# Performance work log

Hardware: AMD Instinct MI355X
Metric: run time of the kernel (lower is better)

The kernel has to match this reference:

```python
import jax, jax.numpy as jnp
import numpy as np
import math

S = 300      # seq_len (timesteps)
P = 10       # n_players
ED = 20      # embedding_dim
D = 512      # d_model = mlp_layers[-1]
H = 8        # nhead
L = 4        # num_layers
FF = 2048    # dim_feedforward
NPID = 600
NPL, NBL, NSL = 121, 1331, 10


def setup_inputs() -> dict:
    key = jax.random.key(0)
    ks = iter(jax.random.split(key, 64))

    def rn(shape, s=0.05):
        return jax.random.normal(next(ks), shape, dtype=jnp.float32) * s

    inp = {
        "player_xs": rn((S, P), 1.0),
        "player_ys": rn((S, P), 1.0),
        "player_hoop_sides": jax.random.uniform(next(ks), (S, P), dtype=jnp.float32),
        "ball_xs": rn((S,), 1.0),
        "ball_ys": rn((S,), 1.0),
        "ball_zs": rn((S,), 1.0),
        "emb_table": rn((NPID, ED)),
        "ball_emb": rn((ED,)),
        "cls_emb": rn((D,)),
        "pW0": rn((128, ED + 3)), "pb0": rn((128,)),
        "pW1": rn((256, 128)), "pb1": rn((256,)),
        "pW2": rn((D, 256)), "pb2": rn((D,)),
        "bW0": rn((128, ED + 3)), "bb0": rn((128,)),
        "bW1": rn((256, 128)), "bb1": rn((256,)),
        "bW2": rn((D, 256)), "bb2": rn((D,)),
        "Wqkv": rn((L, 3 * D, D)), "bqkv": rn((L, 3 * D)),
        "Wo": rn((L, D, D)), "bo": rn((L, D)),
        "W1f": rn((L, FF, D)), "b1f": rn((L, FF)),
        "W2f": rn((L, D, FF)), "b2f": rn((L, D)),
        "g1": jnp.ones((L, D), jnp.float32), "be1": jnp.zeros((L, D), jnp.float32),
        "g2": jnp.ones((L, D), jnp.float32), "be2": jnp.zeros((L, D), jnp.float32),
        "cpW": rn((NPL, D)), "cpb": jnp.zeros((NPL,), jnp.float32),
        "cbW": rn((NBL, D)), "cbb": jnp.zeros((NBL,), jnp.float32),
        "csW": rn((NSL, D)), "csb": jnp.zeros((NSL,), jnp.float32),
        "player_idxs": jax.random.randint(next(ks), (S, P), 0, NPID),
    }
    return inp


def _ln(x, g, b):
    m = x.mean(-1, keepdims=True)
    v = ((x - m) ** 2).mean(-1, keepdims=True)
    return (x - m) / jnp.sqrt(v + 1e-5) * g + b


def _mlp(x, W0, b0, W1, b1, W2, b2):
    x = jax.nn.relu(x @ W0.T + b0)
    x = jax.nn.relu(x @ W1.T + b1)
    return x @ W2.T + b2


def reference(player_xs, player_ys, player_hoop_sides, ball_xs, ball_ys, ball_zs,
              emb_table, ball_emb, cls_emb,
              pW0, pb0, pW1, pb1, pW2, pb2,
              bW0, bb0, bW1, bb1, bW2, bb2,
              Wqkv, bqkv, Wo, bo, W1f, b1f, W2f, b2f,
              g1, be1, g2, be2,
              cpW, cpb, cbW, cbb, csW, csb,
              player_idxs):
    scale = math.sqrt(D)
    # player tokens: [S*P, D]
    pe = emb_table[player_idxs.reshape(-1)]  # sigmoid == "none"
    pin = jnp.concatenate([pe,
                           player_xs.reshape(-1, 1),
                           player_ys.reshape(-1, 1),
                           player_hoop_sides.reshape(-1, 1)], axis=1)
    pf = _mlp(pin, pW0, pb0, pW1, pb1, pW2, pb2) * scale
    # ball tokens: [S, D]
    bin_ = jnp.concatenate([jnp.broadcast_to(ball_emb, (S, ED)),
                            ball_xs[:, None], ball_ys[:, None], ball_zs[:, None]], axis=1)
    bf = _mlp(bin_, bW0, bb0, bW1, bb1, bW2, bb2) * scale
    # [S*P + S + S, D] = [3600, D]
    x = jnp.concatenate([pf, bf, jnp.broadcast_to(cls_emb, (S, D))], axis=0)

    # growing block-causal mask: token j visible to token i iff step(j) <= step(i)
    steps = jnp.concatenate([jnp.repeat(jnp.arange(S), P), jnp.arange(S), jnp.arange(S)])
    mask = jnp.where(steps[None, :] <= steps[:, None], 0.0, -jnp.inf).astype(x.dtype)

    hd = D // H
    sc = 1.0 / math.sqrt(hd)
    for l in range(L):  # post-norm TransformerEncoderLayer, relu activation, dropout=0
        qkv = x @ Wqkv[l].T + bqkv[l]
        q, k, v = jnp.split(qkv, 3, axis=1)
        q = q.reshape(-1, H, hd)
        k = k.reshape(-1, H, hd)
        v = v.reshape(-1, H, hd)
        att = jnp.einsum('qhd,khd->hqk', q, k) * sc + mask
        att = jax.nn.softmax(att, axis=-1)
        o = jnp.einsum('hqk,khd->qhd', att, v).reshape(-1, D)
        x = _ln(x + o @ Wo[l].T + bo[l], g1[l], be1[l])
        ff = jax.nn.relu(x @ W1f[l].T + b1f[l]) @ W2f[l].T + b2f[l]
        x = _ln(x + ff, g2[l], be2[l])

    return (x @ cpW.T + cpb, x @ cbW.T + cbb, x @ csW.T + csb)
```

## Files before the change

### kernel.cpp

```cpp
#include <hip/hip_runtime.h>
#include <hip/hip_bf16.h>

typedef unsigned short u16;
typedef unsigned int u32;
typedef __attribute__((ext_vector_type(8))) short bf16x8;
typedef __attribute__((ext_vector_type(4))) float f32x4;

#define T_TOK 3600
#define D_    512
#define H_    8
#define HD    64
#define NKT   57
#define NQT   113
#define VT_S  3648
#define KSPLIT 8
#define ZSLICE 1843200
#define SQRT512 22.627416997969522f
#define QK_SCALE 0.18033688011112042f

__device__ __forceinline__ u16 f2bf(float f) {
    unsigned int x = __float_as_uint(f);
    unsigned int lsb = (x >> 16) & 1;
    return (u16)((x + 0x7fffu + lsb) >> 16);
}
__device__ __forceinline__ float bf2f(u16 u) {
    return __uint_as_float(((unsigned int)u) << 16);
}
__device__ __forceinline__ u32 cvt_pk_bf16(float a, float b) {
    u32 r;
    asm("v_cvt_pk_bf16_f32 %0, %1, %2" : "=v"(r) : "v"(a), "v"(b));
    return r;
}
__device__ __forceinline__ void async_ld16(const void* g, void* l) {
    __builtin_amdgcn_global_load_lds(
        (const __attribute__((address_space(1))) void*)g,
        (__attribute__((address_space(3))) void*)l, 16, 0, 0);
}
__device__ __forceinline__ int step_of(int i) {
    return (i < 3000) ? (i / 10) : ((i < 3300) ? (i - 3000) : (i - 3300));
}
__device__ __forceinline__ void tile_minmax(int kbase, int& mn, int& mx) {
    int a = kbase, b = min(kbase + 63, T_TOK - 1);
    mn = 0x7fffffff; mx = -1;
    if (a < 3000)              { mn = min(mn, a / 10);              mx = max(mx, min(b, 2999) / 10); }
    if (b >= 3000 && a < 3300) { mn = min(mn, max(a, 3000) - 3000); mx = max(mx, min(b, 3299) - 3000); }
    if (b >= 3300)             { mn = min(mn, max(a, 3300) - 3300); mx = max(mx, b - 3300); }
}

__global__ __launch_bounds__(256) void gather_kernel(
    const float* __restrict__ pxs, const float* __restrict__ pys, const float* __restrict__ phs,
    const float* __restrict__ bxs, const float* __restrict__ bys, const float* __restrict__ bzs,
    const float* __restrict__ emb_table, const float* __restrict__ ball_emb,
    const float* __restrict__ cls_emb, const int* __restrict__ pidx,
    float* __restrict__ IN, float* __restrict__ x, u16* __restrict__ xb)
{
    int g = blockIdx.x * 256 + threadIdx.x;
    if (g < 3300) {
        float* row = IN + g * 24;
        if (g < 3000) {
            int id = pidx[g];
            #pragma unroll
            for (int e = 0; e < 20; e++) row[e] = emb_table[id * 20 + e];
            row[20] = pxs[g]; row[21] = pys[g]; row[22] = phs[g];
        } else {
            int b = g - 3000;
            #pragma unroll
            for (int e = 0; e < 20; e++) row[e] = ball_emb[e];
            row[20] = bxs[b]; row[21] = bys[b]; row[22] = bzs[b];
        }
        row[23] = 0.f;
    }
    for (int i = g; i < 300 * 512; i += 3840) {
        float v = cls_emb[i & 511];
        x[3300 * 512 + i] = v;
        xb[3300 * 512 + i] = f2bf(v);
    }
}

__global__ __launch_bounds__(256) void w2b4_kernel(
    const float* __restrict__ s0, const float* __restrict__ s1,
    const float* __restrict__ s2, const float* __restrict__ s3,
    u16* __restrict__ dst)
{
    int stride = gridDim.x * 256;
    for (int i = blockIdx.x * 256 + threadIdx.x; i < 786432; i += stride) {
        const float4* src;
        int j = i;
        if (j < 196608)      { src = (const float4*)s0; }
        else if (j < 262144) { src = (const float4*)s1; j -= 196608; }
        else if (j < 524288) { src = (const float4*)s2; j -= 262144; }
        else                 { src = (const float4*)s3; j -= 524288; }
        float4 v = src[j];
        ushort4 o;
        o.x = f2bf(v.x); o.y = f2bf(v.y); o.z = f2bf(v.z); o.w = f2bf(v.w);
        reinterpret_cast<ushort4*>(dst)[i] = o;
    }
}

__global__ __launch_bounds__(256) void w2bh_kernel(
    const float* __restrict__ cp, const float* __restrict__ cb,
    const float* __restrict__ cs, const float* __restrict__ bp,
    const float* __restrict__ bb, const float* __restrict__ bs,
    u16* __restrict__ dst, float* __restrict__ bias)
{
    int stride = gridDim.x * 256;
    for (int i = blockIdx.x * 256 + threadIdx.x; i < 187136; i += stride) {
        const float4* src;
        int j = i;
        if (j < 15488)       { src = (const float4*)cp; }
        else if (j < 185856) { src = (const float4*)cb; j -= 15488; }
        else                 { src = (const float4*)cs; j -= 185856; }
        float4 v = src[j];
        ushort4 o;
        o.x = f2bf(v.x); o.y = f2bf(v.y); o.z = f2bf(v.z); o.w = f2bf(v.w);
        reinterpret_cast<ushort4*>(dst)[i] = o;
    }
    int g = blockIdx.x * 256 + threadIdx.x;
    if (g < 1462)
        bias[g] = (g < 121) ? bp[g] : (g < 1452) ? bb[g - 121] : bs[g - 1452];
}

__device__ __forceinline__ void stage_f32(
    const float* __restrict__ src, int nrows, int K, int lda,
    int r0, int kk, int srow, int scg, u16* dst)
{
    u16 tmp[16];
    int rr = r0 + srow;
    if (rr < nrows) {
        if (((lda & 3) == 0) && (kk + scg + 16 <= K)) {
            const float4* p = reinterpret_cast<const float4*>(src + (size_t)rr * lda + kk + scg);
            #pragma unroll
            for (int q = 0; q < 4; q++) {
                float4 v = p[q];
                tmp[q*4+0] = f2bf(v.x); tmp[q*4+1] = f2bf(v.y);
                tmp[q*4+2] = f2bf(v.z); tmp[q*4+3] = f2bf(v.w);
            }
        } else {
            #pragma unroll
            for (int e = 0; e < 16; e++) {
                int kc = kk + scg + e;
                tmp[e] = (kc < K) ? f2bf(src[(size_t)rr * lda + kc]) : (u16)0;
            }
        }
    } else {
        #pragma unroll
        for (int e = 0; e < 16; e++) tmp[e] = 0;
    }
    *reinterpret_cast<bf16x8*>(dst)     = *reinterpret_cast<const bf16x8*>(&tmp[0]);
    *reinterpret_cast<bf16x8*>(dst + 8) = *reinterpret_cast<const bf16x8*>(&tmp[8]);
}

template<int RELU, int DUAL>
__global__ __launch_bounds__(256) void gemm_tok(
    const float* __restrict__ A0, const float* __restrict__ W0p,
    const float* __restrict__ b0p, float* __restrict__ C0,
    const float* __restrict__ A1, const float* __restrict__ W1p,
    const float* __restrict__ b1p, float* __restrict__ C1,
    u16* __restrict__ Cb,
    int M0, int M1, int N, int K, int lda, float scale)
{
    int zz = blockIdx.z;
    int M = zz ? M1 : M0;
    int m0 = blockIdx.x * 128;
    if (m0 >= M) return;
    const float* A = zz ? A1 : A0;
    const float* W = zz ? W1p : W0p;
    const float* bias = zz ? b1p : b0p;
    float* C = zz ? C1 : C0;
    u16* CbL = DUAL ? (zz ? Cb + (size_t)M0 * N : Cb) : nullptr;

    __shared__ u16 As[128][40];
    __shared__ u16 Bs[128][40];
    int t = threadIdx.x;
    int w = t >> 6, l = t & 63;
    int ll = l & 15, lg = l >> 4;
    int wr = w >> 1, wc = w & 1;
    int n0 = blockIdx.y * 128;
    int srow = t >> 1;
    int scg  = (t & 1) * 16;

    f32x4 acc[4][4];
    #pragma unroll
    for (int i = 0; i < 4; i++)
        #pragma unroll
        for (int j = 0; j < 4; j++) acc[i][j] = (f32x4){0.f, 0.f, 0.f, 0.f};

    for (int kk = 0; kk < K; kk += 32) {
        stage_f32(A, M, K, lda, m0, kk, srow, scg, &As[srow][scg]);
        stage_f32(W, N, K, K, n0, kk, srow, scg, &Bs[srow][scg]);
        __syncthreads();
        bf16x8 af[4], bf[4];
        #pragma unroll
        for (int i = 0; i < 4; i++)
            af[i] = *reinterpret_cast<const bf16x8*>(&As[wr*64 + i*16 + ll][lg*8]);
        #pragma unroll
        for (int j = 0; j < 4; j++)
            bf[j] = *reinterpret_cast<const bf16x8*>(&Bs[wc*64 + j*16 + ll][lg*8]);
        #pragma unroll
        for (int i = 0; i < 4; i++)
            #pragma unroll
            for (int j = 0; j < 4; j++)
                acc[i][j] = __builtin_amdgcn_mfma_f32_16x16x32_bf16(af[i], bf[j], acc[i][j], 0, 0, 0);
        __syncthreads();
    }

    float bv[4];
    #pragma unroll
    for (int j = 0; j < 4; j++) {
        int n = n0 + wc*64 + j*16 + ll;
        bv[j] = (n < N) ? bias[n] : 0.f;
    }
    #pragma unroll
    for (int i = 0; i < 4; i++) {
        #pragma unroll
        for (int r = 0; r < 4; r++) {
            int m = m0 + wr*64 + i*16 + lg*4 + r;
            if (m >= M) continue;
            #pragma unroll
            for (int j = 0; j < 4; j++) {
                int n = n0 + wc*64 + j*16 + ll;
                if (n >= N) continue;
                float v = acc[i][j][r] + bv[j];
                if (RELU) v = fmaxf(v, 0.f);
                v *= scale;
                C[(size_t)m * N + n] = v;
                if (DUAL) CbL[(size_t)m * N + n] = f2bf(v);
            }
        }
    }
}

template<int RELU, int BF16OUT, int QSCALE, int SPLITK, int HEADS>
__global__ __launch_bounds__(256) void gemm_async(
    const u16* __restrict__ A, const u16* __restrict__ W,
    const float* __restrict__ bias, void* __restrict__ Cv, float* __restrict__ C1,
    int M, int N, int K, int lda, float scale)
{
    __shared__ u16 As[4096];
    __shared__ u16 Bs[4096];
    int t = threadIdx.x;
    int w = t >> 6, l = t & 63;
    int ll = l & 15, lg = l >> 4;
    int wr = w >> 1, wc = w & 1;
    int m0 = blockIdx.x * 128, n0 = blockIdx.y * 128;
    int srow = l >> 2;
    int skg  = (l & 3) * 8;
    int kz = SPLITK ? blockIdx.z : 0;
    int khalf = SPLITK ? (K >> 1) : K;
    int kbeg = kz * khalf;

    const u16* pa0 = A + (size_t)min(m0 + w * 16 + srow, M - 1) * lda + skg;
    const u16* pa1 = A + (size_t)min(m0 + 64 + w * 16 + srow, M - 1) * lda + skg;
    const u16* pb0 = W + (size_t)min(n0 + w * 16 + srow, N - 1) * K + skg;
    const u16* pb1 = W + (size_t)min(n0 + 64 + w * 16 + srow, N - 1) * K + skg;
    u16* la0 = &As[(w * 16) * 32];
    u16* la1 = &As[(64 + w * 16) * 32];
    u16* lb0 = &Bs[(w * 16) * 32];
    u16* lb1 = &Bs[(64 + w * 16) * 32];

    f32x4 acc[4][4];
    #pragma unroll
    for (int i = 0; i < 4; i++)
        #pragma unroll
        for (int j = 0; j < 4; j++) acc[i][j] = (f32x4){0.f, 0.f, 0.f, 0.f};

    for (int kk = kbeg; kk < kbeg + khalf; kk += 32) {
        async_ld16(pa0 + kk, la0);
        async_ld16(pa1 + kk, la1);
        async_ld16(pb0 + kk, lb0);
        async_ld16(pb1 + kk, lb1);
        __syncthreads();
        bf16x8 af[4], bf[4];
        #pragma unroll
        for (int i = 0; i < 4; i++)
            af[i] = *reinterpret_cast<const bf16x8*>(&As[(wr*64 + i*16 + ll) * 32 + lg*8]);
        #pragma unroll
        for (int j = 0; j < 4; j++)
            bf[j] = *reinterpret_cast<const bf16x8*>(&Bs[(wc*64 + j*16 + ll) * 32 + lg*8]);
        #pragma unroll
        for (int i = 0; i < 4; i++)
            #pragma unroll
            for (int j = 0; j < 4; j++)
                acc[i][j] = __builtin_amdgcn_mfma_f32_16x16x32_bf16(af[i], bf[j], acc[i][j], 0, 0, 0);
        __syncthreads();
    }

    float bv[4];
    #pragma unroll
    for (int j = 0; j < 4; j++) {
        int n = n0 + wc*64 + j*16 + ll;
        bv[j] = (n < N && (!SPLITK || kz == 0)) ? bias[n] : 0.f;
    }
    #pragma unroll
    for (int i = 0; i < 4; i++) {
        #pragma unroll
        for (int r = 0; r < 4; r++) {
            int m = m0 + wr*64 + i*16 + lg*4 + r;
            if (m >= M) continue;
            #pragma unroll
            for (int j = 0; j < 4; j++) {
                int n = n0 + wc*64 + j*16 + ll;
                if (n >= N) continue;
                float v = acc[i][j][r] + bv[j];
                if (RELU) v = fmaxf(v, 0.f);
                v *= scale;
                if (QSCALE && n < 512) v *= QK_SCALE;
                if (HEADS) {
                    float* o = (float*)Cv;
                    if (n < 121)       o[(size_t)m * 121 + n] = v;
                    else if (n < 1452) (o + 435600)[(size_t)m * 1331 + (n - 121)] = v;
                    else               (o + 5227200)[(size_t)m * 10 + (n - 1452)] = v;
                } else if (SPLITK && kz == 1) {
                    C1[(size_t)m * N + n] = v;
                } else if (BF16OUT) {
                    ((u16*)Cv)[(size_t)m * N + n] = f2bf(v);
                } else {
                    ((float*)Cv)[(size_t)m * N + n] = v;
                }
            }
        }
    }
}

__global__ __launch_bounds__(256) void vtrans_kernel(
    const u16* __restrict__ qkvb, u16* __restrict__ vt)
{
    __shared__ u16 tile[64][72];
    int t = threadIdx.x;
    int tok0 = blockIdx.x * 64;
    int h = blockIdx.y;
    {
        int i = t >> 2, c16 = (t & 3) * 16;
        int tok = tok0 + i;
        bf16x8 a = {}, b = {};
        if (tok < T_TOK) {
            const bf16x8* p = reinterpret_cast<const bf16x8*>(qkvb + (size_t)tok * 1536 + 1024 + h * HD + c16);
            a = p[0]; b = p[1];
        }
        *reinterpret_cast<bf16x8*>(&tile[i][c16])     = a;
        *reinterpret_cast<bf16x8*>(&tile[i][c16 + 8]) = b;
    }
    __syncthreads();
    {
        int d = t >> 2, i0 = (t & 3) * 16;
        u16 tt[16];
        #pragma unroll
        for (int e = 0; e < 16; e++) tt[e] = tile[i0 + e][d];
        u16* dst = vt + (size_t)(h * HD + d) * VT_S + tok0 + i0;
        *reinterpret_cast<bf16x8*>(dst)     = *reinterpret_cast<const bf16x8*>(&tt[0]);
        *reinterpret_cast<bf16x8*>(dst + 8) = *reinterpret_cast<const bf16x8*>(&tt[8]);
    }
}

__global__ __launch_bounds__(64) void attn_mfma_kernel(
    const u16* __restrict__ qkvb, const u16* __restrict__ vt,
    u16* __restrict__ Op0, u16* __restrict__ Op1, float* __restrict__ mlpart)
{
    __shared__ u16 plds[2][16][66];
    int l = threadIdx.x;
    int lg = l >> 4, ll = l & 15;
    int bid = blockIdx.x;
    int h = bid & 7;
    int rest = bid >> 3;
    int z = rest / 57;
    int pr = rest - z * 57;

    #pragma unroll 1
    for (int tpart = 0; tpart < 2; tpart++) {
        if (tpart == 1 && pr == 56) break;
        int rank = (tpart == 0) ? pr : 112 - pr;
        int q0 = (112 - rank) * 32;

        bf16x8 qf0[2], qf1[2];
        int sql[2];
        bool qok[2];
        #pragma unroll
        for (int b = 0; b < 2; b++) {
            int qa = q0 + b * 16 + ll;
            qok[b] = qa < T_TOK;
            int qac = min(qa, T_TOK - 1);
            const u16* qrow = qkvb + (size_t)qac * 1536 + h * HD + lg * 8;
            qf0[b] = *reinterpret_cast<const bf16x8*>(qrow);
            qf1[b] = *reinterpret_cast<const bf16x8*>(qrow + 32);
            sql[b] = step_of(qac);
        }
        int sl = max(sql[0], sql[1]), s2 = min(sql[0], sql[1]);
        #pragma unroll
        for (int off = 1; off < 16; off <<= 1) {
            sl = max(sl, __shfl_xor(sl, off));
            s2 = min(s2, __shfl_xor(s2, off));
        }
        int smax = sl, smin = s2;
        int limp[2], limb[2], limc[2];
        #pragma unroll
        for (int b = 0; b < 2; b++) {
            limp[b] = sql[b] * 10 + 9;
            limb[b] = 3000 + sql[b];
            limc[b] = 3300 + sql[b];
        }

        f32x4 oacc[2][4];
        #pragma unroll
        for (int b = 0; b < 2; b++)
            #pragma unroll
            for (int i = 0; i < 4; i++) oacc[b][i] = (f32x4){0.f, 0.f, 0.f, 0.f};
        float m[2] = {-INFINITY, -INFINITY};
        float ls[2] = {0.f, 0.f};

        #pragma unroll 1
        for (int kt = z; kt < NKT; kt += KSPLIT) {
            int kbase = kt * 64;
            int mn, mx;
            tile_minmax(kbase, mn, mx);
            if (mn > smax) continue;
            bool needmask = (mx > smin) || (kbase + 64 > T_TOK);

            bf16x8 kf0[4], kf1[4];
            #pragma unroll
            for (int f = 0; f < 4; f++) {
                int keyc = min(kbase + f * 16 + ll, T_TOK - 1);
                const u16* kr = qkvb + (size_t)keyc * 1536 + 512 + h * HD + lg * 8;
                kf0[f] = *reinterpret_cast<const bf16x8*>(kr);
                kf1[f] = *reinterpret_cast<const bf16x8*>(kr + 32);
            }
            bf16x8 vf0[4], vf1[4];
            #pragma unroll
            for (int i = 0; i < 4; i++) {
                const u16* vr = vt + (size_t)(h * HD + i * 16 + ll) * VT_S + kbase + lg * 8;
                vf0[i] = *reinterpret_cast<const bf16x8*>(vr);
                vf1[i] = *reinterpret_cast<const bf16x8*>(vr + 32);
            }

            f32x4 sfr[2][4];
            __builtin_amdgcn_s_setprio(1);
            #pragma unroll
            for (int f = 0; f < 4; f++) {
                #pragma unroll
                for (int b = 0; b < 2; b++) {
                    f32x4 acc = (f32x4){0.f, 0.f, 0.f, 0.f};
                    acc = __builtin_amdgcn_mfma_f32_16x16x32_bf16(kf0[f], qf0[b], acc, 0, 0, 0);
                    acc = __builtin_amdgcn_mfma_f32_16x16x32_bf16(kf1[f], qf1[b], acc, 0, 0, 0);
                    sfr[b][f] = acc;
                }
            }
            __builtin_amdgcn_s_setprio(0);

            float rmax[2] = {-INFINITY, -INFINITY};
            if (!needmask) {
                #pragma unroll
                for (int f = 0; f < 4; f++)
                    #pragma unroll
                    for (int b = 0; b < 2; b++)
                        #pragma unroll
                        for (int r = 0; r < 4; r++) rmax[b] = fmaxf(rmax[b], sfr[b][f][r]);
            } else {
                #pragma unroll
                for (int f = 0; f < 4; f++)
                    #pragma unroll
                    for (int r = 0; r < 4; r++) {
                        int key = kbase + f * 16 + lg * 4 + r;
                        #pragma unroll
                        for (int b = 0; b < 2; b++) {
                            int lim = (key < 3000) ? limp[b] : ((key < 3300) ? limb[b] : limc[b]);
                            float v = sfr[b][f][r];
                            v = (key <= lim) ? v : -INFINITY;
                            sfr[b][f][r] = v;
                            rmax[b] = fmaxf(rmax[b], v);
                        }
                    }
            }
            if (!qok[0]) rmax[0] = -INFINITY;
            if (!qok[1]) rmax[1] = -INFINITY;
            #pragma unroll
            for (int b = 0; b < 2; b++) {
                rmax[b] = fmaxf(rmax[b], __shfl_xor(rmax[b], 16));
                rmax[b] = fmaxf(rmax[b], __shfl_xor(rmax[b], 32));
            }
            bool upd = (rmax[0] > m[0] + 8.f) || (rmax[1] > m[1] + 8.f);
            if (__any(upd)) {
                #pragma unroll
                for (int b = 0; b < 2; b++) {
                    float mn2 = fmaxf(m[b], rmax[b]);
                    float c = (m[b] == -INFINITY) ? 0.f : exp2f(m[b] - mn2);
                    m[b] = mn2;
                    ls[b] *= c;
                    f32x4 cv;
                    cv[0] = __shfl(c, lg * 4 + 0);
                    cv[1] = __shfl(c, lg * 4 + 1);
                    cv[2] = __shfl(c, lg * 4 + 2);
                    cv[3] = __shfl(c, lg * 4 + 3);
                    #pragma unroll
                    for (int i = 0; i < 4; i++) {
                        oacc[b][i][0] *= cv[0]; oacc[b][i][1] *= cv[1];
                        oacc[b][i][2] *= cv[2]; oacc[b][i][3] *= cv[3];
                    }
                }
            }
            if (!needmask) {
                #pragma unroll
                for (int b = 0; b < 2; b++)
                    #pragma unroll
                    for (int f = 0; f < 4; f++) {
                        float p0 = exp2f(sfr[b][f][0] - m[b]);
                        float p1 = exp2f(sfr[b][f][1] - m[b]);
                        float p2 = exp2f(sfr[b][f][2] - m[b]);
                        float p3 = exp2f(sfr[b][f][3] - m[b]);
                        ls[b] += (p0 + p1) + (p2 + p3);
                        *reinterpret_cast<u32*>(&plds[b][ll][f * 16 + lg * 4])     = cvt_pk_bf16(p0, p1);
                        *reinterpret_cast<u32*>(&plds[b][ll][f * 16 + lg * 4 + 2]) = cvt_pk_bf16(p2, p3);
                    }
            } else {
                #pragma unroll
                for (int b = 0; b < 2; b++)
                    #pragma unroll
                    for (int f = 0; f < 4; f++) {
                        float sv0 = sfr[b][f][0], sv1 = sfr[b][f][1];
                        float sv2 = sfr[b][f][2], sv3 = sfr[b][f][3];
                        float p0 = (sv0 == -INFINITY) ? 0.f : exp2f(sv0 - m[b]);
                        float p1 = (sv1 == -INFINITY) ? 0.f : exp2f(sv1 - m[b]);
                        float p2 = (sv2 == -INFINITY) ? 0.f : exp2f(sv2 - m[b]);
                        float p3 = (sv3 == -INFINITY) ? 0.f : exp2f(sv3 - m[b]);
                        ls[b] += (p0 + p1) + (p2 + p3);
                        *reinterpret_cast<u32*>(&plds[b][ll][f * 16 + lg * 4])     = cvt_pk_bf16(p0, p1);
                        *reinterpret_cast<u32*>(&plds[b][ll][f * 16 + lg * 4 + 2]) = cvt_pk_bf16(p2, p3);
                    }
            }
            __builtin_amdgcn_s_setprio(1);
            #pragma unroll
            for (int b = 0; b < 2; b++) {
                bf16x8 pf0 = *reinterpret_cast<const bf16x8*>(&plds[b][ll][lg * 8]);
                #pragma unroll
                for (int i = 0; i < 4; i++)
                    oacc[b][i] = __builtin_amdgcn_mfma_f32_16x16x32_bf16(pf0, vf0[i], oacc[b][i], 0, 0, 0);
                bf16x8 pf1 = *reinterpret_cast<const bf16x8*>(&plds[b][ll][32 + lg * 8]);
                #pragma unroll
                for (int i = 0; i < 4; i++)
                    oacc[b][i] = __builtin_amdgcn_mfma_f32_16x16x32_bf16(pf1, vf1[i], oacc[b][i], 0, 0, 0);
            }
            __builtin_amdgcn_s_setprio(0);
        }

        #pragma unroll
        for (int b = 0; b < 2; b++) {
            ls[b] += __shfl_xor(ls[b], 16);
            ls[b] += __shfl_xor(ls[b], 32);
        }
        u16* Ob = (z < 5) ? (Op0 + (size_t)z * ZSLICE) : (Op1 + (size_t)(z - 5) * ZSLICE);
        #pragma unroll
        for (int b = 0; b < 2; b++)
            #pragma unroll
            for (int r = 0; r < 4; r++) {
                int q = q0 + b * 16 + lg * 4 + r;
                if (q >= T_TOK) continue;
                size_t ob = ((size_t)h * 3600 + q) * 64;
                #pragma unroll
                for (int i = 0; i < 4; i++)
                    Ob[ob + i * 16 + ll] = f2bf(oacc[b][i][r]);
            }
        if (lg == 0) {
            #pragma unroll
            for (int b = 0; b < 2; b++) {
                int qa = q0 + b * 16 + ll;
                if (qa < T_TOK) {
                    size_t mi = ((size_t)(z * 8 + h) * 3600 + qa) * 2;
                    mlpart[mi]     = m[b];
                    mlpart[mi + 1] = ls[b];
                }
            }
        }
    }
}

__global__ __launch_bounds__(256) void attn_merge_kernel(
    const u16* __restrict__ Op0, const u16* __restrict__ Op1,
    const float* __restrict__ mlpart, u16* __restrict__ obb)
{
    int t = threadIdx.x;
    int h = blockIdx.y;
    int q = blockIdx.x * 64 + (t >> 2);
    if (q >= T_TOK) return;
    int dg = (t & 3) * 16;
    float mz[KSPLIT], lz[KSPLIT];
    #pragma unroll
    for (int zz = 0; zz < KSPLIT; zz++) {
        size_t mi = ((size_t)(zz * 8 + h) * 3600 + q) * 2;
        mz[zz] = mlpart[mi];
        lz[zz] = mlpart[mi + 1];
    }
    float M = -INFINITY;
    #pragma unroll
    for (int zz = 0; zz < KSPLIT; zz++) if (lz[zz] > 0.f) M = fmaxf(M, mz[zz]);
    float wz[KSPLIT], den = 0.f;
    #pragma unroll
    for (int zz = 0; zz < KSPLIT; zz++) {
        wz[zz] = (lz[zz] > 0.f) ? exp2f(mz[zz] - M) : 0.f;
        den += wz[zz] * lz[zz];
    }
    float inv = (den > 0.f) ? 1.f / den : 0.f;
    u16* op = obb + (size_t)q * D_ + h * HD + dg;
    size_t qoff = ((size_t)h * 3600 + q) * 64 + dg;
    #pragma unroll
    for (int e = 0; e < 16; e++) {
        float o = 0.f;
        #pragma unroll
        for (int zz = 0; zz < KSPLIT; zz++) {
            const u16* Ob = (zz < 5) ? (Op0 + (size_t)zz * ZSLICE) : (Op1 + (size_t)(zz - 5) * ZSLICE);
            o += bf2f(Ob[qoff + e]) * wz[zz];
        }
        op[e] = f2bf(o * inv);
    }
}

__global__ __launch_bounds__(256) void add_ln3_kernel(
    float* __restrict__ x, const float* __restrict__ r1, const float* __restrict__ r2,
    const float* __restrict__ g, const float* __restrict__ b,
    u16* __restrict__ xb)
{
    int row = blockIdx.x, t = threadIdx.x;
    size_t base = (size_t)row * D_;
    float v0 = x[base + t] + r1[base + t] + r2[base + t];
    float v1 = x[base + t + 256] + r1[base + t + 256] + r2[base + t + 256];
    float s = v0 + v1, ss = v0 * v0 + v1 * v1;
    #pragma unroll
    for (int off = 32; off > 0; off >>= 1) {
        s  += __shfl_xor(s, off);
        ss += __shfl_xor(ss, off);
    }
    __shared__ float rs[4], rss[4];
    int w = t >> 6;
    if ((t & 63) == 0) { rs[w] = s; rss[w] = ss; }
    __syncthreads();
    s  = rs[0] + rs[1] + rs[2] + rs[3];
    ss = rss[0] + rss[1] + rss[2] + rss[3];
    float mean = s * (1.f / 512.f);
    float var = ss * (1.f / 512.f) - mean * mean;
    float rstd = rsqrtf(var + 1e-5f);
    float o0 = (v0 - mean) * rstd * g[t]       + b[t];
    float o1 = (v1 - mean) * rstd * g[t + 256] + b[t + 256];
    x[base + t]        = o0;
    x[base + t + 256]  = o1;
    xb[base + t]       = f2bf(o0);
    xb[base + t + 256] = f2bf(o1);
}

extern "C" void kernel_launch(void* const* d_in, const int* in_sizes, int n_in,
                              void* d_out, int out_size, void* d_ws, size_t ws_size,
                              hipStream_t stream)
{
    const float* player_xs = (const float*)d_in[0];
    const float* player_ys = (const float*)d_in[1];
    const float* player_hs = (const float*)d_in[2];
    const float* ball_xs   = (const float*)d_in[3];
    const float* ball_ys   = (const float*)d_in[4];
    const float* ball_zs   = (const float*)d_in[5];
    const float* emb_table = (const float*)d_in[6];
    const float* ball_emb  = (const float*)d_in[7];
    const float* cls_emb   = (const float*)d_in[8];
    const float* pW0 = (const float*)d_in[9];   const float* pb0 = (const float*)d_in[10];
    const float* pW1 = (const float*)d_in[11];  const float* pb1 = (const float*)d_in[12];
    const float* pW2 = (const float*)d_in[13];  const float* pb2 = (const float*)d_in[14];
    const float* bW0 = (const float*)d_in[15];  const float* bb0 = (const float*)d_in[16];
    const float* bW1 = (const float*)d_in[17];  const float* bb1 = (const float*)d_in[18];
    const float* bW2 = (const float*)d_in[19];  const float* bb2 = (const float*)d_in[20];
    const float* Wqkv = (const float*)d_in[21]; const float* bqkv = (const float*)d_in[22];
    const float* Wo  = (const float*)d_in[23];  const float* bo  = (const float*)d_in[24];
    const float* W1f = (const float*)d_in[25];  const float* b1f = (const float*)d_in[26];
    const float* W2f = (const float*)d_in[27];  const float* b2f = (const float*)d_in[28];
    const float* g1  = (const float*)d_in[29];  const float* be1 = (const float*)d_in[30];
    const float* g2  = (const float*)d_in[31];  const float* be2 = (const float*)d_in[32];
    const float* cpW = (const float*)d_in[33];  const float* cpb = (const float*)d_in[34];
    const float* cbW = (const float*)d_in[35];  const float* cbb = (const float*)d_in[36];
    const float* csW = (const float*)d_in[37];  const float* csb = (const float*)d_in[38];
    const int* pidx = (const int*)d_in[39];

    float* x    = (float*)d_ws;
    float* big  = x + 1843200;
    float* obr  = big + 7372800;
    float* tmp2 = obr + 1843200;
    u16*   qkvb   = (u16*)big;
    u16*   Op0    = (u16*)(big + 2764800);
    u16*   wbh    = (u16*)(big + 6681600);
    float* bhead  = big + 7100000;
    u16*   ff1b   = (u16*)big;
    float* r2buf  = big + 4000000;
    u16*   obb    = (u16*)obr;
    u16*   xb     = (u16*)(obr + 921600);
    u16*   vt     = (u16*)tmp2;
    float* mlpart = tmp2 + 1000000;
    float* out = (float*)d_out;
    u16* wpack  = (u16*)d_out;
    u16* wqkv_b = wpack;
    u16* wo_b   = wpack + 786432;
    u16* w1f_b  = wpack + 1048576;
    u16* w2f_b  = wpack + 2097152;
    u16* Op1    = wpack + 3145728;
    float* IN = big;
    float* h0 = big + 131072;
    float* h1 = big + 131072 + 460800;

    gather_kernel<<<15, 256, 0, stream>>>(
        player_xs, player_ys, player_hs, ball_xs, ball_ys, ball_zs,
        emb_table, ball_emb, cls_emb, pidx, IN, x, xb);

    gemm_tok<1,0><<<dim3(24, 1, 2), 256, 0, stream>>>(
        IN, pW0, pb0, h0, IN + 3000*24, bW0, bb0, h0 + 3000*128, nullptr,
        3000, 300, 128, 23, 24, 1.f);
    gemm_tok<1,0><<<dim3(24, 2, 2), 256, 0, stream>>>(
        h0, pW1, pb1, h1, h0 + 3000*128, bW1, bb1, h1 + 3000*256, nullptr,
        3000, 300, 256, 128, 128, 1.f);
    gemm_tok<0,1><<<dim3(24, 4, 2), 256, 0, stream>>>(
        h1, pW2, pb2, x, h1 + 3000*256, bW2, bb2, x + 3000*512, xb,
        3000, 300, 512, 256, 256, SQRT512);

    for (int l = 0; l < 4; l++) {
        const float* Wqkv_l = Wqkv + (size_t)l * 1536 * 512;
        const float* bqkv_l = bqkv + (size_t)l * 1536;
        const float* bo_l   = bo   + (size_t)l * 512;
        const float* Wo_l   = Wo   + (size_t)l * 512 * 512;
        const float* W1f_l  = W1f  + (size_t)l * 2048 * 512;
        const float* b1f_l  = b1f  + (size_t)l * 2048;
        const float* W2f_l  = W2f  + (size_t)l * 512 * 2048;
        const float* b2f_l  = b2f  + (size_t)l * 512;

        w2b4_kernel<<<1024, 256, 0, stream>>>(Wqkv_l, Wo_l, W1f_l, W2f_l, wpack);
        gemm_async<0,1,1,0,0><<<dim3(29, 12), 256, 0, stream>>>(xb, wqkv_b, bqkv_l, qkvb, nullptr, 3600, 1536, 512, 512, 1.f);
        vtrans_kernel<<<dim3(57, 8), 256, 0, stream>>>(qkvb, vt);
        attn_mfma_kernel<<<57 * KSPLIT * 8, 64, 0, stream>>>(qkvb, vt, Op0, Op1, mlpart);
        attn_merge_kernel<<<dim3(57, 8), 256, 0, stream>>>(Op0, Op1, mlpart, obb);
        gemm_async<0,0,0,1,0><<<dim3(29, 4, 2), 256, 0, stream>>>(obb, wo_b, bo_l, tmp2, r2buf, 3600, 512, 512, 512, 1.f);
        add_ln3_kernel<<<3600, 256, 0, stream>>>(x, tmp2, r2buf, g1 + (size_t)l * 512, be1 + (size_t)l * 512, xb);
        gemm_async<1,1,0,0,0><<<dim3(29, 16), 256, 0, stream>>>(xb, w1f_b, b1f_l, ff1b, nullptr, 3600, 2048, 512, 512, 1.f);
        gemm_async<0,0,0,1,0><<<dim3(29, 4, 2), 256, 0, stream>>>(ff1b, w2f_b, b2f_l, tmp2, r2buf, 3600, 512, 2048, 2048, 1.f);
        add_ln3_kernel<<<3600, 256, 0, stream>>>(x, tmp2, r2buf, g2 + (size_t)l * 512, be2 + (size_t)l * 512, xb);
    }

    w2bh_kernel<<<732, 256, 0, stream>>>(cpW, cbW, csW, cpb, cbb, csb, wbh, bhead);
    gemm_async<0,0,0,0,1><<<dim3(29, 12), 256, 0, stream>>>(xb, wbh, bhead, out, nullptr, 3600, 1462, 512, 512, 1.f);
}
```

Before: 922.0 us.

## Fuse V transpose into QKV GEMM epilogue and widen attention query tiles to 64

The QKV GEMM now writes the V columns directly into the transposed vt buffer, which removes the separate vtrans kernel. The weight-conversion kernel zeroes the vt padding columns instead. The attention kernel now handles 64 queries per tile (four 16-row blocks) rather than 32, so each loaded K/V tile is reused across more queries and fewer blocks are launched. K fragments are loaded per 16-key group inside the score loop to limit register pressure. The trade-offs are more registers and LDS per wave and fewer blocks to occupy the device.

After: 1.005 ms. 9.0% more time.

```diff
diff --git a/kernel.cpp b/kernel.cpp
--- a/kernel.cpp
+++ b/kernel.cpp
@@ -11,7 +11,6 @@
 #define H_    8
 #define HD    64
 #define NKT   57
-#define NQT   113
 #define VT_S  3648
 #define KSPLIT 8
 #define ZSLICE 1843200
@@ -80,7 +79,7 @@
 __global__ __launch_bounds__(256) void w2b4_kernel(
     const float* __restrict__ s0, const float* __restrict__ s1,
     const float* __restrict__ s2, const float* __restrict__ s3,
-    u16* __restrict__ dst)
+    u16* __restrict__ dst, u16* __restrict__ vt)
 {
     int stride = gridDim.x * 256;
     for (int i = blockIdx.x * 256 + threadIdx.x; i < 786432; i += stride) {
@@ -95,6 +94,10 @@
         o.x = f2bf(v.x); o.y = f2bf(v.y); o.z = f2bf(v.z); o.w = f2bf(v.w);
         reinterpret_cast<ushort4*>(dst)[i] = o;
     }
+    for (int i = blockIdx.x * 256 + threadIdx.x; i < 512 * 64; i += stride) {
+        int row = i >> 6, c = i & 63;
+        if (c < 48) vt[(size_t)row * VT_S + 3600 + c] = 0;
+    }
 }
 
 __global__ __launch_bounds__(256) void w2bh_kernel(
@@ -230,11 +233,11 @@
     }
 }
 
-template<int RELU, int BF16OUT, int QSCALE, int SPLITK, int HEADS>
+template<int RELU, int BF16OUT, int QSCALE, int SPLITK, int HEADS, int VTOUT>
 __global__ __launch_bounds__(256) void gemm_async(
     const u16* __restrict__ A, const u16* __restrict__ W,
     const float* __restrict__ bias, void* __restrict__ Cv, float* __restrict__ C1,
-    int M, int N, int K, int lda, float scale)
+    u16* __restrict__ vtp, int M, int N, int K, int lda, float scale)
 {
     __shared__ u16 As[4096];
     __shared__ u16 Bs[4096];
@@ -293,62 +296,59 @@
     }
     #pragma unroll
     for (int i = 0; i < 4; i++) {
-        #pragma unroll
-        for (int r = 0; r < 4; r++) {
-            int m = m0 + wr*64 + i*16 + lg*4 + r;
-            if (m >= M) continue;
+        if (VTOUT) {
             #pragma unroll
             for (int j = 0; j < 4; j++) {
                 int n = n0 + wc*64 + j*16 + ll;
-                if (n >= N) continue;
-                float v = acc[i][j][r] + bv[j];
-                if (RELU) v = fmaxf(v, 0.f);
-                v *= scale;
-                if (QSCALE && n < 512) v *= QK_SCALE;
-                if (HEADS) {
-                    float* o = (float*)Cv;
-                    if (n < 121)       o[(size_t)m * 121 + n] = v;
-                    else if (n < 1452) (o + 435600)[(size_t)m * 1331 + (n - 121)] = v;
-                    else               (o + 5227200)[(size_t)m * 10 + (n - 1452)] = v;
-                } else if (SPLITK && kz == 1) {
-                    C1[(size_t)m * N + n] = v;
-                } else if (BF16OUT) {
-                    ((u16*)Cv)[(size_t)m * N + n] = f2bf(v);
+                int mb = m0 + wr*64 + i*16 + lg*4;
+                if (n >= 1024) {
+                    if (mb < T_TOK) {
+                        ushort4 o;
+                        o.x = f2bf(acc[i][j][0] + bv[j]);
+                        o.y = f2bf(acc[i][j][1] + bv[j]);
+                        o.z = f2bf(acc[i][j][2] + bv[j]);
+                        o.w = f2bf(acc[i][j][3] + bv[j]);
+                        *reinterpret_cast<ushort4*>(vtp + (size_t)(n - 1024) * VT_S + mb) = o;
+                    }
                 } else {
-                    ((float*)Cv)[(size_t)m * N + n] = v;
+                    #pragma unroll
+                    for (int r = 0; r < 4; r++) {
+                        int mm = mb + r;
+                        if (mm >= M) continue;
+                        float v = acc[i][j][r] + bv[j];
+                        if (n < 512) v *= QK_SCALE;
+                        ((u16*)Cv)[(size_t)mm * N + n] = f2bf(v);
+                    }
                 }
             }
-        }
-    }
-}
-
-__global__ __launch_bounds__(256) void vtrans_kernel(
-    const u16* __restrict__ qkvb, u16* __restrict__ vt)
-{
-    __shared__ u16 tile[64][72];
-    int t = threadIdx.x;
-    int tok0 = blockIdx.x * 64;
-    int h = blockIdx.y;
-    {
-        int i = t >> 2, c16 = (t & 3) * 16;
-        int tok = tok0 + i;
-        bf16x8 a = {}, b = {};
-        if (tok < T_TOK) {
-            const bf16x8* p = reinterpret_cast<const bf16x8*>(qkvb + (size_t)tok * 1536 + 1024 + h * HD + c16);
-            a = p[0]; b = p[1];
-        }
-        *reinterpret_cast<bf16x8*>(&tile[i][c16])     = a;
-        *reinterpret_cast<bf16x8*>(&tile[i][c16 + 8]) = b;
-    }
-    __syncthreads();
-    {
-        int d = t >> 2, i0 = (t & 3) * 16;
-        u16 tt[16];
-        #pragma unroll
-        for (int e = 0; e < 16; e++) tt[e] = tile[i0 + e][d];
-        u16* dst = vt + (size_t)(h * HD + d) * VT_S + tok0 + i0;
-        *reinterpret_cast<bf16x8*>(dst)     = *reinterpret_cast<const bf16x8*>(&tt[0]);
-        *reinterpret_cast<bf16x8*>(dst + 8) = *reinterpret_cast<const bf16x8*>(&tt[8]);
+        } else {
+            #pragma unroll
+            for (int r = 0; r < 4; r++) {
+                int m = m0 + wr*64 + i*16 + lg*4 + r;
+                if (m >= M) continue;
+                #pragma unroll
+                for (int j = 0; j < 4; j++) {
+                    int n = n0 + wc*64 + j*16 + ll;
+                    if (n >= N) continue;
+                    float v = acc[i][j][r] + bv[j];
+                    if (RELU) v = fmaxf(v, 0.f);
+                    v *= scale;
+                    if (QSCALE && n < 512) v *= QK_SCALE;
+                    if (HEADS) {
+                        float* o = (float*)Cv;
+                        if (n < 121)       o[(size_t)m * 121 + n] = v;
+                        else if (n < 1452) (o + 435600)[(size_t)m * 1331 + (n - 121)] = v;
+                        else               (o + 5227200)[(size_t)m * 10 + (n - 1452)] = v;
+                    } else if (SPLITK && kz == 1) {
+                        C1[(size_t)m * N + n] = v;
+                    } else if (BF16OUT) {
+                        ((u16*)Cv)[(size_t)m * N + n] = f2bf(v);
+                    } else {
+                        ((float*)Cv)[(size_t)m * N + n] = v;
+                    }
+                }
+            }
+        }
     }
 }
 
@@ -356,26 +356,26 @@
     const u16* __restrict__ qkvb, const u16* __restrict__ vt,
     u16* __restrict__ Op0, u16* __restrict__ Op1, float* __restrict__ mlpart)
 {
-    __shared__ u16 plds[2][16][66];
+    __shared__ u16 plds[4][16][66];
     int l = threadIdx.x;
     int lg = l >> 4, ll = l & 15;
     int bid = blockIdx.x;
     int h = bid & 7;
     int rest = bid >> 3;
-    int z = rest / 57;
-    int pr = rest - z * 57;
+    int z = rest / 29;
+    int pr = rest - z * 29;
 
     #pragma unroll 1
     for (int tpart = 0; tpart < 2; tpart++) {
-        if (tpart == 1 && pr == 56) break;
-        int rank = (tpart == 0) ? pr : 112 - pr;
-        int q0 = (112 - rank) * 32;
-
-        bf16x8 qf0[2], qf1[2];
-        int sql[2];
-        bool qok[2];
-        #pragma unroll
-        for (int b = 0; b < 2; b++) {
+        if (tpart == 1 && pr == 28) break;
+        int rank = (tpart == 0) ? pr : 56 - pr;
+        int q0 = (56 - rank) * 64;
+
+        bf16x8 qf0[4], qf1[4];
+        int sql[4];
+        bool qok[4];
+        #pragma unroll
+        for (int b = 0; b < 4; b++) {
             int qa = q0 + b * 16 + ll;
             qok[b] = qa < T_TOK;
             int qac = min(qa, T_TOK - 1);
@@ -384,28 +384,29 @@
             qf1[b] = *reinterpret_cast<const bf16x8*>(qrow + 32);
             sql[b] = step_of(qac);
         }
-        int sl = max(sql[0], sql[1]), s2 = min(sql[0], sql[1]);
+        int sl = max(max(sql[0], sql[1]), max(sql[2], sql[3]));
+        int s2 = min(min(sql[0], sql[1]), min(sql[2], sql[3]));
         #pragma unroll
         for (int off = 1; off < 16; off <<= 1) {
             sl = max(sl, __shfl_xor(sl, off));
             s2 = min(s2, __shfl_xor(s2, off));
         }
         int smax = sl, smin = s2;
-        int limp[2], limb[2], limc[2];
-        #pragma unroll
-        for (int b = 0; b < 2; b++) {
+        int limp[4], limb[4], limc[4];
+        #pragma unroll
+        for (int b = 0; b < 4; b++) {
             limp[b] = sql[b] * 10 + 9;
             limb[b] = 3000 + sql[b];
             limc[b] = 3300 + sql[b];
         }
 
-        f32x4 oacc[2][4];
-        #pragma unroll
-        for (int b = 0; b < 2; b++)
+        f32x4 oacc[4][4];
+        #pragma unroll
+        for (int b = 0; b < 4; b++)
             #pragma unroll
             for (int i = 0; i < 4; i++) oacc[b][i] = (f32x4){0.f, 0.f, 0.f, 0.f};
-        float m[2] = {-INFINITY, -INFINITY};
-        float ls[2] = {0.f, 0.f};
+        float m[4] = {-INFINITY, -INFINITY, -INFINITY, -INFINITY};
+        float ls[4] = {0.f, 0.f, 0.f, 0.f};
 
         #pragma unroll 1
         for (int kt = z; kt < NKT; kt += KSPLIT) {
@@ -415,14 +416,6 @@
             if (mn > smax) continue;
             bool needmask = (mx > smin) || (kbase + 64 > T_TOK);
 
-            bf16x8 kf0[4], kf1[4];
-            #pragma unroll
-            for (int f = 0; f < 4; f++) {
-                int keyc = min(kbase + f * 16 + ll, T_TOK - 1);
-                const u16* kr = qkvb + (size_t)keyc * 1536 + 512 + h * HD + lg * 8;
-                kf0[f] = *reinterpret_cast<const bf16x8*>(kr);
-                kf1[f] = *reinterpret_cast<const bf16x8*>(kr + 32);
-            }
             bf16x8 vf0[4], vf1[4];
             #pragma unroll
             for (int i = 0; i < 4; i++) {
@@ -431,26 +424,30 @@
                 vf1[i] = *reinterpret_cast<const bf16x8*>(vr + 32);
             }
 
-            f32x4 sfr[2][4];
-            __builtin_amdgcn_s_setprio(1);
+            f32x4 sfr[4][4];
             #pragma unroll
             for (int f = 0; f < 4; f++) {
-                #pragma unroll
-                for (int b = 0; b < 2; b++) {
+                int keyc = min(kbase + f * 16 + ll, T_TOK - 1);
+                const u16* kr = qkvb + (size_t)keyc * 1536 + 512 + h * HD + lg * 8;
+                bf16x8 kf0 = *reinterpret_cast<const bf16x8*>(kr);
+                bf16x8 kf1 = *reinterpret_cast<const bf16x8*>(kr + 32);
+                __builtin_amdgcn_s_setprio(1);
+                #pragma unroll
+                for (int b = 0; b < 4; b++) {
                     f32x4 acc = (f32x4){0.f, 0.f, 0.f, 0.f};
-                    acc = __builtin_amdgcn_mfma_f32_16x16x32_bf16(kf0[f], qf0[b], acc, 0, 0, 0);
-                    acc = __builtin_amdgcn_mfma_f32_16x16x32_bf16(kf1[f], qf1[b], acc, 0, 0, 0);
+                    acc = __builtin_amdgcn_mfma_f32_16x16x32_bf16(kf0, qf0[b], acc, 0, 0, 0);
+                    acc = __builtin_amdgcn_mfma_f32_16x16x32_bf16(kf1, qf1[b], acc, 0, 0, 0);
                     sfr[b][f] = acc;
                 }
-            }
-            __builtin_amdgcn_s_setprio(0);
-
-            float rmax[2] = {-INFINITY, -INFINITY};
+                __builtin_amdgcn_s_setprio(0);
+            }
+
+            float rmax[4] = {-INFINITY, -INFINITY, -INFINITY, -INFINITY};
             if (!needmask) {
                 #pragma unroll
                 for (int f = 0; f < 4; f++)
                     #pragma unroll
-                    for (int b = 0; b < 2; b++)
+                    for (int b = 0; b < 4; b++)
                         #pragma unroll
                         for (int r = 0; r < 4; r++) rmax[b] = fmaxf(rmax[b], sfr[b][f][r]);
             } else {
@@ -460,7 +457,7 @@
                     for (int r = 0; r < 4; r++) {
                         int key = kbase + f * 16 + lg * 4 + r;
                         #pragma unroll
-                        for (int b = 0; b < 2; b++) {
+                        for (int b = 0; b < 4; b++) {
                             int lim = (key < 3000) ? limp[b] : ((key < 3300) ? limb[b] : limc[b]);
                             float v = sfr[b][f][r];
                             v = (key <= lim) ? v : -INFINITY;
@@ -469,17 +466,18 @@
                         }
                     }
             }
-            if (!qok[0]) rmax[0] = -INFINITY;
-            if (!qok[1]) rmax[1] = -INFINITY;
-            #pragma unroll
-            for (int b = 0; b < 2; b++) {
+            #pragma unroll
+            for (int b = 0; b < 4; b++) {
+                if (!qok[b]) rmax[b] = -INFINITY;
                 rmax[b] = fmaxf(rmax[b], __shfl_xor(rmax[b], 16));
                 rmax[b] = fmaxf(rmax[b], __shfl_xor(rmax[b], 32));
             }
-            bool upd = (rmax[0] > m[0] + 8.f) || (rmax[1] > m[1] + 8.f);
+            bool upd = false;
+            #pragma unroll
+            for (int b = 0; b < 4; b++) upd = upd || (rmax[b] > m[b] + 8.f);
             if (__any(upd)) {
                 #pragma unroll
-                for (int b = 0; b < 2; b++) {
+                for (int b = 0; b < 4; b++) {
                     float mn2 = fmaxf(m[b], rmax[b]);
                     float c = (m[b] == -INFINITY) ? 0.f : exp2f(m[b] - mn2);
                     m[b] = mn2;
@@ -498,7 +496,7 @@
             }
             if (!needmask) {
                 #pragma unroll
-                for (int b = 0; b < 2; b++)
+                for (int b = 0; b < 4; b++)
                     #pragma unroll
                     for (int f = 0; f < 4; f++) {
                         float p0 = exp2f(sfr[b][f][0] - m[b]);
@@ -511,7 +509,7 @@
                     }
             } else {
                 #pragma unroll
-                for (int b = 0; b < 2; b++)
+                for (int b = 0; b < 4; b++)
                     #pragma unroll
                     for (int f = 0; f < 4; f++) {
                         float sv0 = sfr[b][f][0], sv1 = sfr[b][f][1];
@@ -527,7 +525,7 @@
             }
             __builtin_amdgcn_s_setprio(1);
             #pragma unroll
-            for (int b = 0; b < 2; b++) {
+            for (int b = 0; b < 4; b++) {
                 bf16x8 pf0 = *reinterpret_cast<const bf16x8*>(&plds[b][ll][lg * 8]);
                 #pragma unroll
                 for (int i = 0; i < 4; i++)
@@ -541,13 +539,13 @@
         }
 
         #pragma unroll
-        for (int b = 0; b < 2; b++) {
+        for (int b = 0; b < 4; b++) {
             ls[b] += __shfl_xor(ls[b], 16);
             ls[b] += __shfl_xor(ls[b], 32);
         }
         u16* Ob = (z < 5) ? (Op0 + (size_t)z * ZSLICE) : (Op1 + (size_t)(z - 5) * ZSLICE);
         #pragma unroll
-        for (int b = 0; b < 2; b++)
+        for (int b = 0; b < 4; b++)
             #pragma unroll
             for (int r = 0; r < 4; r++) {
                 int q = q0 + b * 16 + lg * 4 + r;
@@ -559,7 +557,7 @@
             }
         if (lg == 0) {
             #pragma unroll
-            for (int b = 0; b < 2; b++) {
+            for (int b = 0; b < 4; b++) {
                 int qa = q0 + b * 16 + ll;
                 if (qa < T_TOK) {
                     size_t mi = ((size_t)(z * 8 + h) * 3600 + qa) * 2;
@@ -722,18 +720,17 @@
         const float* W2f_l  = W2f  + (size_t)l * 512 * 2048;
         const float* b2f_l  = b2f  + (size_t)l * 512;
 
-        w2b4_kernel<<<1024, 256, 0, stream>>>(Wqkv_l, Wo_l, W1f_l, W2f_l, wpack);
-        gemm_async<0,1,1,0,0><<<dim3(29, 12), 256, 0, stream>>>(xb, wqkv_b, bqkv_l, qkvb, nullptr, 3600, 1536, 512, 512, 1.f);
-        vtrans_kernel<<<dim3(57, 8), 256, 0, stream>>>(qkvb, vt);
-        attn_mfma_kernel<<<57 * KSPLIT * 8, 64, 0, stream>>>(qkvb, vt, Op0, Op1, mlpart);
+        w2b4_kernel<<<1024, 256, 0, stream>>>(Wqkv_l, Wo_l, W1f_l, W2f_l, wpack, vt);
+        gemm_async<0,1,1,0,0,1><<<dim3(29, 12), 256, 0, stream>>>(xb, wqkv_b, bqkv_l, qkvb, nullptr, vt, 3600, 1536, 512, 512, 1.f);
+        attn_mfma_kernel<<<29 * 8 * 8, 64, 0, stream>>>(qkvb, vt, Op0, Op1, mlpart);
         attn_merge_kernel<<<dim3(57, 8), 256, 0, stream>>>(Op0, Op1, mlpart, obb);
-        gemm_async<0,0,0,1,0><<<dim3(29, 4, 2), 256, 0, stream>>>(obb, wo_b, bo_l, tmp2, r2buf, 3600, 512, 512, 512, 1.f);
+        gemm_async<0,0,0,1,0,0><<<dim3(29, 4, 2), 256, 0, stream>>>(obb, wo_b, bo_l, tmp2, r2buf, nullptr, 3600, 512, 512, 512, 1.f);
         add_ln3_kernel<<<3600, 256, 0, stream>>>(x, tmp2, r2buf, g1 + (size_t)l * 512, be1 + (size_t)l * 512, xb);
-        gemm_async<1,1,0,0,0><<<dim3(29, 16), 256, 0, stream>>>(xb, w1f_b, b1f_l, ff1b, nullptr, 3600, 2048, 512, 512, 1.f);
-        gemm_async<0,0,0,1,0><<<dim3(29, 4, 2), 256, 0, stream>>>(ff1b, w2f_b, b2f_l, tmp2, r2buf, 3600, 512, 2048, 2048, 1.f);
+        gemm_async<1,1,0,0,0,0><<<dim3(29, 16), 256, 0, stream>>>(xb, w1f_b, b1f_l, ff1b, nullptr, nullptr, 3600, 2048, 512, 512, 1.f);
+        gemm_async<0,0,0,1,0,0><<<dim3(29, 4, 2), 256, 0, stream>>>(ff1b, w2f_b, b2f_l, tmp2, r2buf, nullptr, 3600, 512, 2048, 2048, 1.f);
         add_ln3_kernel<<<3600, 256, 0, stream>>>(x, tmp2, r2buf, g2 + (size_t)l * 512, be2 + (size_t)l * 512, xb);
     }
 
     w2bh_kernel<<<732, 256, 0, stream>>>(cpW, cbW, csW, cpb, cbb, csb, wbh, bhead);
-    gemm_async<0,0,0,0,1><<<dim3(29, 12), 256, 0, stream>>>(xb, wbh, bhead, out, nullptr, 3600, 1462, 512, 512, 1.f);
-}
+    gemm_async<0,0,0,0,1,0><<<dim3(29, 12), 256, 0, stream>>>(xb, wbh, bhead, out, nullptr, nullptr, 3600, 1462, 512, 512, 1.f);
+}
```
